# Optimization experiments

Hardware: AMD Instinct MI355X
Metric: run time of the kernel (lower is better)

The kernel has to match this reference:

```python
import jax, jax.numpy as jnp
import numpy as np

N = 100000      # nodes
E = 1600000     # edges (avg degree 16)
D_IN, D_H, D_OUT = 128, 128, 64


def setup_inputs() -> dict:
    key = jax.random.key(0)
    k1, k2, k3, k4 = jax.random.split(key, 4)
    x = jax.random.normal(k1, (N, D_IN), dtype=jnp.float32)
    edge_index = jax.random.randint(k2, (2, E), 0, N, dtype=jnp.int32)
    W1 = jax.random.normal(k3, (D_IN, D_H), dtype=jnp.float32) * (1.0 / np.sqrt(D_IN))
    b1 = jnp.zeros((D_H,), dtype=jnp.float32)
    W2 = jax.random.normal(k4, (D_H, D_OUT), dtype=jnp.float32) * (1.0 / np.sqrt(D_H))
    b2 = jnp.zeros((D_OUT,), dtype=jnp.float32)
    return {"x": x, "edge_index": edge_index, "W1": W1, "b1": b1, "W2": W2, "b2": b2}


def _gcn_conv(x, src, dst, W, b):
    """PyG GCNConv: out = D^{-1/2} (A + I) D^{-1/2} (x W) + b."""
    n = x.shape[0]
    h = x @ W  # [N, D_out] — transform first, then aggregate (PyG order)
    loops = jnp.arange(n, dtype=src.dtype)
    src_f = jnp.concatenate([src, loops])
    dst_f = jnp.concatenate([dst, loops])
    deg = jax.ops.segment_sum(jnp.ones_like(dst_f, dtype=h.dtype), dst_f, num_segments=n)
    dinv = jax.lax.rsqrt(deg)  # deg >= 1 due to self-loops
    norm = dinv[src_f] * dinv[dst_f]            # [E+N]
    msg = h[src_f] * norm[:, None]              # [E+N, D_out] gather
    out = jax.ops.segment_sum(msg, dst_f, num_segments=n)  # scatter-add
    return out + b


def reference(x, edge_index, W1, b1, W2, b2):
    src, dst = edge_index[0], edge_index[1]
    h = jax.nn.relu(_gcn_conv(x, src, dst, W1, b1))
    o = _gcn_conv(h, src, dst, W2, b2)
    return jax.nn.log_softmax(o, axis=1)
```

## Files before the change

kernel.cpp:

```cpp
#include <hip/hip_runtime.h>
#include <hip/hip_bf16.h>

typedef __hip_bfloat16 bf16;
typedef short short8 __attribute__((ext_vector_type(8)));
typedef float f32x4 __attribute__((ext_vector_type(4)));

#define NPB 256
#define MAXBUK 1024

__device__ __forceinline__ float bf2f_raw(unsigned short u) {
    unsigned x = ((unsigned)u) << 16; float f; __builtin_memcpy(&f, &x, 4); return f;
}
__device__ __forceinline__ unsigned short f2bf_raw(float f) {
    unsigned u; __builtin_memcpy(&u, &f, 4);
    u += 0x7FFFu + ((u >> 16) & 1u);
    return (unsigned short)(u >> 16);
}
__device__ __forceinline__ float lo_f(unsigned u) {
    unsigned x = u << 16; float f; __builtin_memcpy(&f, &x, 4); return f;
}
__device__ __forceinline__ float hi_f(unsigned u) {
    unsigned x = u & 0xffff0000u; float f; __builtin_memcpy(&f, &x, 4); return f;
}


__global__ __launch_bounds__(1024) void sniff_kernel(const unsigned short* __restrict__ w,
                                                     int nshorts, int* __restrict__ flag) {
    __shared__ int red[1024];
    const int t = threadIdx.x;
    int c = 0;
    for (int i = t; i < nshorts; i += 1024) {
        unsigned e = (w[i] >> 7) & 0xFFu;
        if (e >= 140u || (e >= 1u && e <= 40u)) c++;
    }
    red[t] = c;
    __syncthreads();
    for (int o = 512; o > 0; o >>= 1) {
        if (t < o) red[t] += red[t + o];
        __syncthreads();
    }
    if (t == 0) *flag = (red[0] > nshorts / 8) ? 1 : 0;
}


__global__ __launch_bounds__(256) void prep_kernel(const void* __restrict__ W1p,
                                                   const void* __restrict__ W2p,
                                                   const void* __restrict__ b1p,
                                                   const void* __restrict__ b2p,
                                                   unsigned short* __restrict__ WB1,
                                                   unsigned short* __restrict__ WB2,
                                                   float* __restrict__ b1f,
                                                   float* __restrict__ b2f,
                                                   const int* __restrict__ flag) {
    const int isf32 = *flag;
    const int t = blockIdx.x * 256 + threadIdx.x;
    const int T1 = 16384, T2 = 8192;
    if (t < T1) {
        int j = t & 7, l = (t >> 3) & 63, f = t >> 9;
        int n = f >> 2, kk = f & 3;
        int k = kk * 32 + (l >> 4) * 8 + j;
        int col = n * 16 + (l & 15);
        WB1[t] = isf32 ? f2bf_raw(((const float*)W1p)[k * 128 + col])
                       : ((const unsigned short*)W1p)[k * 128 + col];
    } else if (t < T1 + T2) {
        int o = t - T1;
        int j = o & 7, l = (o >> 3) & 63, f = o >> 9;
        int n = f >> 2, kk = f & 3;
        int k = kk * 32 + (l >> 4) * 8 + j;
        int col = n * 16 + (l & 15);
        WB2[o] = isf32 ? f2bf_raw(((const float*)W2p)[k * 64 + col])
                       : ((const unsigned short*)W2p)[k * 64 + col];
    } else if (t < T1 + T2 + 128) {
        int o = t - T1 - T2;
        b1f[o] = isf32 ? ((const float*)b1p)[o] : bf2f_raw(((const unsigned short*)b1p)[o]);
    } else if (t < T1 + T2 + 192) {
        int o = t - T1 - T2 - 128;
        b2f[o] = isf32 ? ((const float*)b2p)[o] : bf2f_raw(((const unsigned short*)b2p)[o]);
    }
}


__global__ __launch_bounds__(256) void ms_count_kernel(const int* __restrict__ dst,
                                                       int* __restrict__ bktcnt,
                                                       int E, int nbuk) {
    __shared__ int cnt[MAXBUK];
    const int t = threadIdx.x;
    const int e0 = blockIdx.x * 4096;
    const int e1 = min(E, e0 + 4096);
    for (int b = t; b < nbuk; b += 256) cnt[b] = 0;
    __syncthreads();
    for (int e = e0 + t; e < e1; e += 256) atomicAdd(&cnt[dst[e] >> 8], 1);
    __syncthreads();
    for (int b = t; b < nbuk; b += 256) {
        int c = cnt[b];
        if (c) atomicAdd(&bktcnt[b], c);
    }
}

__global__ __launch_bounds__(1024) void bscan_kernel(const int* __restrict__ bktcnt,
                                                     int* __restrict__ bofs,
                                                     int* __restrict__ bcur,
                                                     int* __restrict__ rofs,
                                                     int nbuk, int n, int total) {
    __shared__ int ps[1024];
    const int t = threadIdx.x;
    int v = (t < nbuk) ? bktcnt[t] : 0;
    ps[t] = v;
    __syncthreads();
    for (int o = 1; o < 1024; o <<= 1) {
        int u = (t >= o) ? ps[t - o] : 0;
        __syncthreads();
        ps[t] += u;
        __syncthreads();
    }
    if (t < nbuk) {
        int ex = ps[t] - v;
        bofs[t] = ex;
        bcur[t] = ex;
    }
    if (t == 0) {
        bofs[nbuk] = total;
        rofs[n] = total;
    }
}

__global__ __launch_bounds__(256) void ms_scatter_kernel(const int* __restrict__ src,
                                                         const int* __restrict__ dst,
                                                         int* __restrict__ bcur,
                                                         unsigned* __restrict__ packed,
                                                         int E, int nbuk) {
    __shared__ int cnt[MAXBUK];
    __shared__ int gbase[MAXBUK];
    const int t = threadIdx.x;
    const int e0 = blockIdx.x * 4096;
    const int e1 = min(E, e0 + 4096);
    for (int b = t; b < nbuk; b += 256) cnt[b] = 0;
    __syncthreads();
    for (int e = e0 + t; e < e1; e += 256) atomicAdd(&cnt[dst[e] >> 8], 1);
    __syncthreads();
    for (int b = t; b < nbuk; b += 256) {
        int c = cnt[b];
        gbase[b] = c ? atomicAdd(&bcur[b], c) : 0;
        cnt[b] = 0;
    }
    __syncthreads();
    for (int e = e0 + t; e < e1; e += 256) {
        int d = dst[e];
        int b = d >> 8;
        int r = atomicAdd(&cnt[b], 1);
        packed[gbase[b] + r] = ((unsigned)(d & 255) << 24) | (unsigned)src[e];
    }
}

__global__ __launch_bounds__(256) void csr_fine2_kernel(const unsigned* __restrict__ packed,
                                                        const int* __restrict__ bofs,
                                                        int* __restrict__ rofs,
                                                        float* __restrict__ dinv,
                                                        int* __restrict__ csrc, int n) {
    __shared__ int cnt2[NPB];
    __shared__ int cur[NPB];
    const int t = threadIdx.x;
    const int b = blockIdx.x;
    const int node0 = b << 8;
    const int nn = min(NPB, n - node0);
    cnt2[t] = 0;
    __syncthreads();
    const int beg = bofs[b], end = bofs[b + 1];
    for (int i = beg + t; i < end; i += 256) atomicAdd(&cnt2[packed[i] >> 24], 1);
    __syncthreads();
    int c = cnt2[t];
    cur[t] = c;
    __syncthreads();
    for (int o = 1; o < 256; o <<= 1) {
        int u = (t >= o) ? cur[t - o] : 0;
        __syncthreads();
        cur[t] += u;
        __syncthreads();
    }
    const int base = beg + cur[t] - c;
    if (t < nn) {
        rofs[node0 + t] = base;
        dinv[node0 + t] = rsqrtf((float)(c + 1));
    }
    __syncthreads();
    cur[t] = base;
    __syncthreads();
    for (int i = beg + t; i < end; i += 256) {
        unsigned u = packed[i];
        int pos = atomicAdd(&cur[u >> 24], 1);
        csrc[pos] = (int)(u & 0xFFFFFFu);
    }
}

__global__ __launch_bounds__(256) void wsrc_kernel(const int* __restrict__ csrc,
                                                   const float* __restrict__ dinv,
                                                   float* __restrict__ wsrc, int E) {
    int i = blockIdx.x * 256 + threadIdx.x;
    if (i < E) wsrc[i] = dinv[csrc[i]];
}


__global__ __launch_bounds__(256) void gemm1_mfma(const void* __restrict__ Xp,
                                                  const unsigned short* __restrict__ WB1,
                                                  unsigned short* __restrict__ H, int nrows,
                                                  const int* __restrict__ flag) {
    __shared__ __align__(16) unsigned short Xs[128 * 136];
    __shared__ __align__(16) unsigned short Cs[128 * 68];
    const int t = threadIdx.x;
    const int r0 = blockIdx.x * 128;
    const int isf32 = *flag;

    if (isf32) {
        const float4* Xg = (const float4*)Xp;
        #pragma unroll
        for (int i = 0; i < 16; ++i) {
            int idx = t + 256 * i;
            int row = idx >> 5, c4 = idx & 31;
            float4 v = {0.f, 0.f, 0.f, 0.f};
            if (r0 + row < nrows) v = Xg[(size_t)(r0 + row) * 32 + c4];
            unsigned lo = (unsigned)f2bf_raw(v.x) | ((unsigned)f2bf_raw(v.y) << 16);
            unsigned hi = (unsigned)f2bf_raw(v.z) | ((unsigned)f2bf_raw(v.w) << 16);
            *reinterpret_cast<uint2*>(&Xs[row * 136 + c4 * 4]) = make_uint2(lo, hi);
        }
    } else {
        const uint4* Xg = (const uint4*)Xp;
        #pragma unroll
        for (int i = 0; i < 8; ++i) {
            int idx = t + 256 * i;
            int row = idx >> 4, c8 = idx & 15;
            uint4 v = {0u, 0u, 0u, 0u};
            if (r0 + row < nrows) v = Xg[(size_t)(r0 + row) * 16 + c8];
            *reinterpret_cast<uint4*>(&Xs[row * 136 + c8 * 8]) = v;
        }
    }
    __syncthreads();

    const int lane = t & 63, w = t >> 6;
    const int m0 = w * 32;
    short8 a[2][4];
    #pragma unroll
    for (int rt = 0; rt < 2; ++rt)
        #pragma unroll
        for (int kk = 0; kk < 4; ++kk)
            a[rt][kk] = *reinterpret_cast<const short8*>(
                &Xs[(m0 + rt * 16 + (lane & 15)) * 136 + kk * 32 + (lane >> 4) * 8]);

    for (int p = 0; p < 2; ++p) {
        short8 b[4][4];
        #pragma unroll
        for (int n = 0; n < 4; ++n)
            #pragma unroll
            for (int kk = 0; kk < 4; ++kk)
                b[n][kk] = *reinterpret_cast<const short8*>(
                    WB1 + (size_t)(((p * 4 + n) * 4 + kk) * 64 + lane) * 8);
        f32x4 acc[2][4];
        #pragma unroll
        for (int rt = 0; rt < 2; ++rt)
            #pragma unroll
            for (int n = 0; n < 4; ++n) {
                acc[rt][n] = (f32x4){0.f, 0.f, 0.f, 0.f};
                #pragma unroll
                for (int kk = 0; kk < 4; ++kk)
                    acc[rt][n] = __builtin_amdgcn_mfma_f32_16x16x32_bf16(
                        a[rt][kk], b[n][kk], acc[rt][n], 0, 0, 0);
            }
        if (p) __syncthreads();
        #pragma unroll
        for (int rt = 0; rt < 2; ++rt)
            #pragma unroll
            for (int n = 0; n < 4; ++n)
                #pragma unroll
                for (int r = 0; r < 4; ++r) {
                    int row = m0 + rt * 16 + (lane >> 4) * 4 + r;
                    Cs[row * 68 + n * 16 + (lane & 15)] = f2bf_raw(acc[rt][n][r]);
                }
        __syncthreads();
        #pragma unroll
        for (int i = 0; i < 8; ++i) {
            int idx = t + 256 * i;
            int row = idx >> 4, c4 = idx & 15;
            if (r0 + row < nrows) {
                uint2 v = *reinterpret_cast<const uint2*>(&Cs[row * 68 + c4 * 4]);
                *reinterpret_cast<uint2*>(H + (size_t)(r0 + row) * 128 + p * 64 + c4 * 4) = v;
            }
        }
        if (!p) __syncthreads();
    }
}


__device__ __forceinline__ void acc8(float* acc, uint4 v, float w) {
    acc[0] = fmaf(w, lo_f(v.x), acc[0]); acc[1] = fmaf(w, hi_f(v.x), acc[1]);
    acc[2] = fmaf(w, lo_f(v.y), acc[2]); acc[3] = fmaf(w, hi_f(v.y), acc[3]);
    acc[4] = fmaf(w, lo_f(v.z), acc[4]); acc[5] = fmaf(w, hi_f(v.z), acc[5]);
    acc[6] = fmaf(w, lo_f(v.w), acc[6]); acc[7] = fmaf(w, hi_f(v.w), acc[7]);
}

template <bool RELU_BIAS>
__global__ __launch_bounds__(256) void agg128_v3(const uint4* __restrict__ H4,
                                                 const int* __restrict__ rofs,
                                                 const int* __restrict__ csrc,
                                                 const float* __restrict__ wsrc,
                                                 const float* __restrict__ dinv,
                                                 const float* __restrict__ biasf,
                                                 uint4* __restrict__ G4, int n) {
    const int lane = threadIdx.x & 63;
    const int g = lane >> 4;
    const int sub = lane & 15;
    const int node = blockIdx.x * 4 + (threadIdx.x >> 6);
    if (node >= n) return;
    const float di = dinv[node];

    float acc[8];
    {
        const float ws = (g == 0) ? di * di : 0.f;
        uint4 v = H4[(size_t)node * 16 + sub];
        acc[0] = ws * lo_f(v.x); acc[1] = ws * hi_f(v.x);
        acc[2] = ws * lo_f(v.y); acc[3] = ws * hi_f(v.y);
        acc[4] = ws * lo_f(v.z); acc[5] = ws * hi_f(v.z);
        acc[6] = ws * lo_f(v.w); acc[7] = ws * hi_f(v.w);
    }

    int j = rofs[node];
    const int end = rofs[node + 1];

    for (; j + 7 < end; j += 8) {
        int s0 = csrc[j + g];
        int s1 = csrc[j + 4 + g];
        float w0 = di * wsrc[j + g];
        float w1 = di * wsrc[j + 4 + g];
        uint4 v0 = H4[(size_t)s0 * 16 + sub];
        uint4 v1 = H4[(size_t)s1 * 16 + sub];
        acc8(acc, v0, w0);
        acc8(acc, v1, w1);
    }
    for (; j + 3 < end; j += 4) {
        int s0 = csrc[j + g];
        float w0 = di * wsrc[j + g];
        uint4 v0 = H4[(size_t)s0 * 16 + sub];
        acc8(acc, v0, w0);
    }
    if (j + g < end) {
        int s0 = csrc[j + g];
        float w0 = di * wsrc[j + g];
        uint4 v0 = H4[(size_t)s0 * 16 + sub];
        acc8(acc, v0, w0);
    }

    #pragma unroll
    for (int i = 0; i < 8; ++i) {
        acc[i] += __shfl_xor(acc[i], 16, 64);
        acc[i] += __shfl_xor(acc[i], 32, 64);
    }

    if (g == 0) {
        if (RELU_BIAS) {
            const float4* b4 = (const float4*)biasf;
            float4 blo = b4[sub * 2], bhi = b4[sub * 2 + 1];
            acc[0] = fmaxf(acc[0] + blo.x, 0.f);
            acc[1] = fmaxf(acc[1] + blo.y, 0.f);
            acc[2] = fmaxf(acc[2] + blo.z, 0.f);
            acc[3] = fmaxf(acc[3] + blo.w, 0.f);
            acc[4] = fmaxf(acc[4] + bhi.x, 0.f);
            acc[5] = fmaxf(acc[5] + bhi.y, 0.f);
            acc[6] = fmaxf(acc[6] + bhi.z, 0.f);
            acc[7] = fmaxf(acc[7] + bhi.w, 0.f);
        }
        uint4 o;
        o.x = (unsigned)f2bf_raw(acc[0]) | ((unsigned)f2bf_raw(acc[1]) << 16);
        o.y = (unsigned)f2bf_raw(acc[2]) | ((unsigned)f2bf_raw(acc[3]) << 16);
        o.z = (unsigned)f2bf_raw(acc[4]) | ((unsigned)f2bf_raw(acc[5]) << 16);
        o.w = (unsigned)f2bf_raw(acc[6]) | ((unsigned)f2bf_raw(acc[7]) << 16);
        G4[(size_t)node * 16 + sub] = o;
    }
}


__global__ __launch_bounds__(256) void gemm2_mfma(const unsigned short* __restrict__ X,
                                                  const unsigned short* __restrict__ WB2,
                                                  const float* __restrict__ b2f,
                                                  void* __restrict__ OUTv, int nrows,
                                                  const int* __restrict__ flag) {
    __shared__ __align__(16) unsigned short Xs[128 * 136];
    const int t = threadIdx.x;
    const int r0 = blockIdx.x * 128;
    const int outf32 = *flag;

    const uint4* Xg = (const uint4*)X;
    #pragma unroll
    for (int i = 0; i < 8; ++i) {
        int idx = t + 256 * i;
        int row = idx >> 4, c8 = idx & 15;
        uint4 v = {0u, 0u, 0u, 0u};
        if (r0 + row < nrows) v = Xg[(size_t)(r0 + row) * 16 + c8];
        *reinterpret_cast<uint4*>(&Xs[row * 136 + c8 * 8]) = v;
    }
    __syncthreads();

    const int lane = t & 63, w = t >> 6;
    const int m0 = w * 32;
    short8 a[2][4];
    #pragma unroll
    for (int rt = 0; rt < 2; ++rt)
        #pragma unroll
        for (int kk = 0; kk < 4; ++kk)
            a[rt][kk] = *reinterpret_cast<const short8*>(
                &Xs[(m0 + rt * 16 + (lane & 15)) * 136 + kk * 32 + (lane >> 4) * 8]);

    short8 b[4][4];
    #pragma unroll
    for (int n = 0; n < 4; ++n)
        #pragma unroll
        for (int kk = 0; kk < 4; ++kk)
            b[n][kk] = *reinterpret_cast<const short8*>(
                WB2 + (size_t)((n * 4 + kk) * 64 + lane) * 8);

    f32x4 acc[2][4];
    #pragma unroll
    for (int rt = 0; rt < 2; ++rt)
        #pragma unroll
        for (int n = 0; n < 4; ++n) {
            acc[rt][n] = (f32x4){0.f, 0.f, 0.f, 0.f};
            #pragma unroll
            for (int kk = 0; kk < 4; ++kk)
                acc[rt][n] = __builtin_amdgcn_mfma_f32_16x16x32_bf16(
                    a[rt][kk], b[n][kk], acc[rt][n], 0, 0, 0);
        }

    float bc[4];
    #pragma unroll
    for (int n = 0; n < 4; ++n) bc[n] = b2f[n * 16 + (lane & 15)];
    #pragma unroll
    for (int rt = 0; rt < 2; ++rt)
        #pragma unroll
        for (int n = 0; n < 4; ++n)
            #pragma unroll
            for (int r = 0; r < 4; ++r) acc[rt][n][r] += bc[n];

    float lse[2][4];
    #pragma unroll
    for (int rt = 0; rt < 2; ++rt)
        #pragma unroll
        for (int r = 0; r < 4; ++r) {
            float m = fmaxf(fmaxf(acc[rt][0][r], acc[rt][1][r]),
                            fmaxf(acc[rt][2][r], acc[rt][3][r]));
            #pragma unroll
            for (int o = 1; o < 16; o <<= 1) m = fmaxf(m, __shfl_xor(m, o, 64));
            float s = __expf(acc[rt][0][r] - m) + __expf(acc[rt][1][r] - m) +
                      __expf(acc[rt][2][r] - m) + __expf(acc[rt][3][r] - m);
            #pragma unroll
            for (int o = 1; o < 16; o <<= 1) s += __shfl_xor(s, o, 64);
            lse[rt][r] = m + __logf(s);
        }

    const int colb = lane & 15, q = lane >> 4;
    #pragma unroll
    for (int rt = 0; rt < 2; ++rt)
        #pragma unroll
        for (int r = 0; r < 4; ++r) {
            int grow = r0 + m0 + rt * 16 + q * 4 + r;
            if (grow < nrows) {
                if (outf32) {
                    float* Of = (float*)OUTv;
                    #pragma unroll
                    for (int n = 0; n < 4; ++n)
                        Of[(size_t)grow * 64 + n * 16 + colb] = acc[rt][n][r] - lse[rt][r];
                } else {
                    unsigned short* Ob = (unsigned short*)OUTv;
                    #pragma unroll
                    for (int n = 0; n < 4; ++n)
                        Ob[(size_t)grow * 64 + n * 16 + colb] = f2bf_raw(acc[rt][n][r] - lse[rt][r]);
                }
            }
        }
}


extern "C" void kernel_launch(void* const* d_in, const int* in_sizes, int n_in,
                              void* d_out, int out_size, void* d_ws, size_t ws_size,
                              hipStream_t stream) {
    const void* x  = d_in[0];
    const int*  ei = (const int*)d_in[1];
    const void* W1 = d_in[2];
    const void* b1 = d_in[3];
    const void* W2 = d_in[4];
    const void* b2 = d_in[5];

    const int N = in_sizes[0] / 128;
    const int E = in_sizes[1] / 2;
    const int* src = ei;
    const int* dst = ei + E;
    const int NBUK = (N + NPB - 1) / NPB;

    char* p = (char*)d_ws;
    auto alloc = [&](size_t bytes) { char* q = p; p += (bytes + 255) & ~255ull; return q; };
    int*   flag   = (int*)  alloc(4);
    int*   rofs   = (int*)  alloc((size_t)(N + 1) * 4);
    float* dinv   = (float*)alloc((size_t)N * 4);
    int*   bktcnt = (int*)  alloc((size_t)NBUK * 4);
    int*   bofs   = (int*)  alloc((size_t)(NBUK + 1) * 4);
    int*   bcur   = (int*)  alloc((size_t)NBUK * 4);
    float* b1f    = (float*)alloc(128 * 4);
    float* b2f    = (float*)alloc(64 * 4);
    unsigned short* WB1 = (unsigned short*)alloc(16384 * 2);
    unsigned short* WB2 = (unsigned short*)alloc(8192 * 2);
    unsigned* big = (unsigned*)alloc((size_t)N * 128 * 2);
    unsigned* packed = (unsigned*)d_out;
    float*    wsrc   = (float*)d_out;
    int*      csrc   = (int*)d_out + E;
    unsigned* g1 = (unsigned*)d_in[0];
    (void)ws_size; (void)n_in; (void)out_size;

    hipMemsetAsync(bktcnt, 0, (size_t)NBUK * 4, stream);
    sniff_kernel<<<1, 1024, 0, stream>>>((const unsigned short*)W1, in_sizes[2], flag);
    prep_kernel<<<97, 256, 0, stream>>>(W1, W2, b1, b2, WB1, WB2, b1f, b2f, flag);
    const int MSB = (E + 4095) / 4096;
    ms_count_kernel<<<MSB, 256, 0, stream>>>(dst, bktcnt, E, NBUK);
    bscan_kernel<<<1, 1024, 0, stream>>>(bktcnt, bofs, bcur, rofs, NBUK, N, E);
    ms_scatter_kernel<<<MSB, 256, 0, stream>>>(src, dst, bcur, packed, E, NBUK);
    csr_fine2_kernel<<<NBUK, 256, 0, stream>>>(packed, bofs, rofs, dinv, csrc, N);
    wsrc_kernel<<<(E + 255) / 256, 256, 0, stream>>>(csrc, dinv, wsrc, E);

    const int GB = (N + 127) / 128;
    gemm1_mfma<<<GB, 256, 0, stream>>>(x, WB1, (unsigned short*)big, N, flag);
    agg128_v3<true><<<(N + 3) / 4, 256, 0, stream>>>((const uint4*)big, rofs, csrc, wsrc, dinv, b1f, (uint4*)g1, N);
    agg128_v3<false><<<(N + 3) / 4, 256, 0, stream>>>((const uint4*)g1, rofs, csrc, wsrc, dinv, nullptr, (uint4*)big, N);
    gemm2_mfma<<<GB, 256, 0, stream>>>((const unsigned short*)big, WB2, b2f, d_out, N, flag);
}
```

Measured before the change: 326.6 us.

## Restructure aggregation loop: 16-edge unrolled gathers, packed node metadata, packed FMA

```diff
diff --git a/kernel.cpp b/kernel.cpp
--- a/kernel.cpp
+++ b/kernel.cpp
@@ -4,6 +4,7 @@
 typedef __hip_bfloat16 bf16;
 typedef short short8 __attribute__((ext_vector_type(8)));
 typedef float f32x4 __attribute__((ext_vector_type(4)));
+typedef float f32x2 __attribute__((ext_vector_type(2)));
 
 #define NPB 256
 #define MAXBUK 1024
@@ -100,8 +101,7 @@
 __global__ __launch_bounds__(1024) void bscan_kernel(const int* __restrict__ bktcnt,
                                                      int* __restrict__ bofs,
                                                      int* __restrict__ bcur,
-                                                     int* __restrict__ rofs,
-                                                     int nbuk, int n, int total) {
+                                                     int nbuk, int total) {
     __shared__ int ps[1024];
     const int t = threadIdx.x;
     int v = (t < nbuk) ? bktcnt[t] : 0;
@@ -118,10 +118,7 @@
         bofs[t] = ex;
         bcur[t] = ex;
     }
-    if (t == 0) {
-        bofs[nbuk] = total;
-        rofs[n] = total;
-    }
+    if (t == 0) bofs[nbuk] = total;
 }
 
 __global__ __launch_bounds__(256) void ms_scatter_kernel(const int* __restrict__ src,
@@ -154,7 +151,7 @@
 
 __global__ __launch_bounds__(256) void csr_fine2_kernel(const unsigned* __restrict__ packed,
                                                         const int* __restrict__ bofs,
-                                                        int* __restrict__ rofs,
+                                                        uint2* __restrict__ nmeta,
                                                         float* __restrict__ dinv,
                                                         int* __restrict__ csrc, int n) {
     __shared__ int cnt2[NPB];
@@ -179,7 +176,7 @@
     }
     const int base = beg + cur[t] - c;
     if (t < nn) {
-        rofs[node0 + t] = base;
+        nmeta[node0 + t] = make_uint2((unsigned)base, (unsigned)c);
         dinv[node0 + t] = rsqrtf((float)(c + 1));
     }
     __syncthreads();
@@ -289,19 +286,19 @@
 }
 
 
-__device__ __forceinline__ void acc8(float* acc, uint4 v, float w) {
-    acc[0] = fmaf(w, lo_f(v.x), acc[0]); acc[1] = fmaf(w, hi_f(v.x), acc[1]);
-    acc[2] = fmaf(w, lo_f(v.y), acc[2]); acc[3] = fmaf(w, hi_f(v.y), acc[3]);
-    acc[4] = fmaf(w, lo_f(v.z), acc[4]); acc[5] = fmaf(w, hi_f(v.z), acc[5]);
-    acc[6] = fmaf(w, lo_f(v.w), acc[6]); acc[7] = fmaf(w, hi_f(v.w), acc[7]);
+__device__ __forceinline__ void acc8v(f32x2* acc, uint4 v, float w) {
+    f32x2 wv = {w, w};
+    acc[0] += (f32x2){lo_f(v.x), hi_f(v.x)} * wv;
+    acc[1] += (f32x2){lo_f(v.y), hi_f(v.y)} * wv;
+    acc[2] += (f32x2){lo_f(v.z), hi_f(v.z)} * wv;
+    acc[3] += (f32x2){lo_f(v.w), hi_f(v.w)} * wv;
 }
 
 template <bool RELU_BIAS>
-__global__ __launch_bounds__(256) void agg128_v3(const uint4* __restrict__ H4,
-                                                 const int* __restrict__ rofs,
+__global__ __launch_bounds__(256) void agg128_v4(const uint4* __restrict__ H4,
+                                                 const uint2* __restrict__ nmeta,
                                                  const int* __restrict__ csrc,
                                                  const float* __restrict__ wsrc,
-                                                 const float* __restrict__ dinv,
                                                  const float* __restrict__ biasf,
                                                  uint4* __restrict__ G4, int n) {
     const int lane = threadIdx.x & 63;
@@ -309,68 +306,68 @@
     const int sub = lane & 15;
     const int node = blockIdx.x * 4 + (threadIdx.x >> 6);
     if (node >= n) return;
-    const float di = dinv[node];
-
-    float acc[8];
+    const uint2 meta = nmeta[node];
+    const int base = (int)meta.x;
+    const int cnt = (int)meta.y;
+    const int end = base + cnt;
+    const float di = rsqrtf((float)(cnt + 1));
+
+    f32x2 acc[4];
     {
         const float ws = (g == 0) ? di * di : 0.f;
         uint4 v = H4[(size_t)node * 16 + sub];
-        acc[0] = ws * lo_f(v.x); acc[1] = ws * hi_f(v.x);
-        acc[2] = ws * lo_f(v.y); acc[3] = ws * hi_f(v.y);
-        acc[4] = ws * lo_f(v.z); acc[5] = ws * hi_f(v.z);
-        acc[6] = ws * lo_f(v.w); acc[7] = ws * hi_f(v.w);
-    }
-
-    int j = rofs[node];
-    const int end = rofs[node + 1];
-
-    for (; j + 7 < end; j += 8) {
-        int s0 = csrc[j + g];
-        int s1 = csrc[j + 4 + g];
-        float w0 = di * wsrc[j + g];
-        float w1 = di * wsrc[j + 4 + g];
+        acc[0] = (f32x2){ws * lo_f(v.x), ws * hi_f(v.x)};
+        acc[1] = (f32x2){ws * lo_f(v.y), ws * hi_f(v.y)};
+        acc[2] = (f32x2){ws * lo_f(v.z), ws * hi_f(v.z)};
+        acc[3] = (f32x2){ws * lo_f(v.w), ws * hi_f(v.w)};
+    }
+
+    for (int j = base; j < end; j += 16) {
+        const int lim = end - 1;
+        int i0 = j + g, i1 = j + 4 + g, i2 = j + 8 + g, i3 = j + 12 + g;
+        int c0 = min(i0, lim), c1 = min(i1, lim), c2 = min(i2, lim), c3 = min(i3, lim);
+        int s0 = csrc[c0], s1 = csrc[c1], s2 = csrc[c2], s3 = csrc[c3];
+        float w0 = (i0 <= lim) ? di * wsrc[c0] : 0.f;
+        float w1 = (i1 <= lim) ? di * wsrc[c1] : 0.f;
+        float w2 = (i2 <= lim) ? di * wsrc[c2] : 0.f;
+        float w3 = (i3 <= lim) ? di * wsrc[c3] : 0.f;
         uint4 v0 = H4[(size_t)s0 * 16 + sub];
         uint4 v1 = H4[(size_t)s1 * 16 + sub];
-        acc8(acc, v0, w0);
-        acc8(acc, v1, w1);
-    }
-    for (; j + 3 < end; j += 4) {
-        int s0 = csrc[j + g];
-        float w0 = di * wsrc[j + g];
-        uint4 v0 = H4[(size_t)s0 * 16 + sub];
-        acc8(acc, v0, w0);
-    }
-    if (j + g < end) {
-        int s0 = csrc[j + g];
-        float w0 = di * wsrc[j + g];
-        uint4 v0 = H4[(size_t)s0 * 16 + sub];
-        acc8(acc, v0, w0);
-    }
-
+        uint4 v2 = H4[(size_t)s2 * 16 + sub];
+        uint4 v3 = H4[(size_t)s3 * 16 + sub];
+        acc8v(acc, v0, w0);
+        acc8v(acc, v1, w1);
+        acc8v(acc, v2, w2);
+        acc8v(acc, v3, w3);
+    }
+
+    float a8[8];
+    #pragma unroll
+    for (int i = 0; i < 4; ++i) { a8[2 * i] = acc[i].x; a8[2 * i + 1] = acc[i].y; }
     #pragma unroll
     for (int i = 0; i < 8; ++i) {
-        acc[i] += __shfl_xor(acc[i], 16, 64);
-        acc[i] += __shfl_xor(acc[i], 32, 64);
+        a8[i] += __shfl_xor(a8[i], 16, 64);
+        a8[i] += __shfl_xor(a8[i], 32, 64);
     }
 
     if (g == 0) {
         if (RELU_BIAS) {
             const float4* b4 = (const float4*)biasf;
             float4 blo = b4[sub * 2], bhi = b4[sub * 2 + 1];
-            acc[0] = fmaxf(acc[0] + blo.x, 0.f);
-            acc[1] = fmaxf(acc[1] + blo.y, 0.f);
-            acc[2] = fmaxf(acc[2] + blo.z, 0.f);
-            acc[3] = fmaxf(acc[3] + blo.w, 0.f);
-            acc[4] = fmaxf(acc[4] + bhi.x, 0.f);
-            acc[5] = fmaxf(acc[5] + bhi.y, 0.f);
-            acc[6] = fmaxf(acc[6] + bhi.z, 0.f);
-            acc[7] = fmaxf(acc[7] + bhi.w, 0.f);
+            a8[0] = fmaxf(a8[0] + blo.x, 0.f);
+            a8[1] = fmaxf(a8[1] + blo.y, 0.f);
+            a8[2] = fmaxf(a8[2] + blo.z, 0.f);
+            a8[3] = fmaxf(a8[3] + blo.w, 0.f);
+            a8[4] = fmaxf(a8[4] + bhi.x, 0.f);
+            a8[5] = fmaxf(a8[5] + bhi.y, 0.f);
+            a8[6] = fmaxf(a8[6] + bhi.z, 0.f);
+            a8[7] = fmaxf(a8[7] + bhi.w, 0.f);
         }
         uint4 o;
-        o.x = (unsigned)f2bf_raw(acc[0]) | ((unsigned)f2bf_raw(acc[1]) << 16);
-        o.y = (unsigned)f2bf_raw(acc[2]) | ((unsigned)f2bf_raw(acc[3]) << 16);
-        o.z = (unsigned)f2bf_raw(acc[4]) | ((unsigned)f2bf_raw(acc[5]) << 16);
-        o.w = (unsigned)f2bf_raw(acc[6]) | ((unsigned)f2bf_raw(acc[7]) << 16);
+        o.x = (unsigned)f2bf_raw(a8[0]) | ((unsigned)f2bf_raw(a8[1]) << 16);
+        o.y = (unsigned)f2bf_raw(a8[2]) | ((unsigned)f2bf_raw(a8[3]) << 16);
+        o.z = (unsigned)f2bf_raw(a8[4]) | ((unsigned)f2bf_raw(a8[5]) << 16);
+        o.w = (unsigned)f2bf_raw(a8[6]) | ((unsigned)f2bf_raw(a8[7]) << 16);
         G4[(size_t)node * 16 + sub] = o;
     }
 }
@@ -495,7 +492,7 @@
     char* p = (char*)d_ws;
     auto alloc = [&](size_t bytes) { char* q = p; p += (bytes + 255) & ~255ull; return q; };
     int*   flag   = (int*)  alloc(4);
-    int*   rofs   = (int*)  alloc((size_t)(N + 1) * 4);
+    uint2* nmeta  = (uint2*)alloc((size_t)N * 8);
     float* dinv   = (float*)alloc((size_t)N * 4);
     int*   bktcnt = (int*)  alloc((size_t)NBUK * 4);
     int*   bofs   = (int*)  alloc((size_t)(NBUK + 1) * 4);
@@ -516,14 +513,14 @@
     prep_kernel<<<97, 256, 0, stream>>>(W1, W2, b1, b2, WB1, WB2, b1f, b2f, flag);
     const int MSB = (E + 4095) / 4096;
     ms_count_kernel<<<MSB, 256, 0, stream>>>(dst, bktcnt, E, NBUK);
-    bscan_kernel<<<1, 1024, 0, stream>>>(bktcnt, bofs, bcur, rofs, NBUK, N, E);
+    bscan_kernel<<<1, 1024, 0, stream>>>(bktcnt, bofs, bcur, NBUK, E);
     ms_scatter_kernel<<<MSB, 256, 0, stream>>>(src, dst, bcur, packed, E, NBUK);
-    csr_fine2_kernel<<<NBUK, 256, 0, stream>>>(packed, bofs, rofs, dinv, csrc, N);
+    csr_fine2_kernel<<<NBUK, 256, 0, stream>>>(packed, bofs, nmeta, dinv, csrc, N);
     wsrc_kernel<<<(E + 255) / 256, 256, 0, stream>>>(csrc, dinv, wsrc, E);
 
     const int GB = (N + 127) / 128;
     gemm1_mfma<<<GB, 256, 0, stream>>>(x, WB1, (unsigned short*)big, N, flag);
-    agg128_v3<true><<<(N + 3) / 4, 256, 0, stream>>>((const uint4*)big, rofs, csrc, wsrc, dinv, b1f, (uint4*)g1, N);
-    agg128_v3<false><<<(N + 3) / 4, 256, 0, stream>>>((const uint4*)g1, rofs, csrc, wsrc, dinv, nullptr, (uint4*)big, N);
+    agg128_v4<true><<<(N + 3) / 4, 256, 0, stream>>>((const uint4*)big, nmeta, csrc, wsrc, b1f, (uint4*)g1, N);
+    agg128_v4<false><<<(N + 3) / 4, 256, 0, stream>>>((const uint4*)g1, nmeta, csrc, wsrc, nullptr, (uint4*)big, N);
     gemm2_mfma<<<GB, 256, 0, stream>>>((const unsigned short*)big, WB2, b2f, d_out, N, flag);
 }
```

Result: slower. 334.6 us (+2.4%).
